# Performance work log

Measured on AMD Instinct MI355X. Metric: run time of the kernel, lower is better.

Reference implementation:

```python
import jax, jax.numpy as jnp
import numpy as np

N = 100_000       # nodes
DEG = 16          # avg degree (fixed here)
E = N * DEG       # edges
IN_F, HID, OUT_F = 64, 32, 16
K, DIM = 3, 2     # n_kernels, pseudo-coordinate dim


def setup_inputs() -> dict:
    key = jax.random.key(0)
    k1, k2, k3, k4, k5, k6, k7 = jax.random.split(key, 7)
    row_ptr = jnp.arange(N + 1, dtype=jnp.int64) * DEG          # CSR offsets, fixed degree
    col_idx = jax.random.randint(k1, (E,), 0, N, dtype=jnp.int64)
    input_feature = jax.random.normal(k2, (N, IN_F), dtype=jnp.float32)
    p = jax.random.uniform(k3, (E, DIM), dtype=jnp.float32)      # pseudo-coordinates per edge
    mu = jax.random.normal(k4, (K, DIM), dtype=jnp.float32)
    sigma = jax.random.uniform(k5, (K, DIM), dtype=jnp.float32, minval=0.5, maxval=1.5)
    W1 = jax.random.normal(k6, (K, IN_F, HID), dtype=jnp.float32) * (1.0 / np.sqrt(IN_F))
    W2 = jax.random.normal(k7, (K, HID, OUT_F), dtype=jnp.float32) * (1.0 / np.sqrt(HID))
    return {"row_ptr": row_ptr, "col_idx": col_idx, "input_feature": input_feature,
            "p": p, "mu": mu, "sigma": sigma, "W1": W1, "W2": W2}


def _edge_gaussians(p, mu, sigma):
    # w[e,k] = exp(-0.5 * sum_d ((p[e,d]-mu[k,d])/sigma[k,d])^2)   [E,K]
    diff = p[:, None, :] - mu[None, :, :]                 # [E,K,D]
    inv_var = 1.0 / (sigma * sigma)                       # [K,D]
    return jnp.exp(-0.5 * jnp.sum(diff * diff * inv_var[None], axis=-1))


def _gmm_conv(row_ptr, col_idx, dst, x, gauss, W):
    # per-kernel linear transform first (dense GEMM), then irregular gather+scatter
    xW = jnp.einsum('nf,kfh->nkh', x, W)                  # [N,K,H]
    msg = jnp.einsum('ek,ekh->eh', gauss, xW[col_idx])    # gather + mix kernels  [E,H]
    n_nodes = row_ptr.shape[0] - 1
    return jax.ops.segment_sum(msg, dst, num_segments=n_nodes)  # scatter-add to dst rows


def reference(row_ptr, col_idx, input_feature, p, mu, sigma, W1, W2):
    n_nodes = row_ptr.shape[0] - 1
    deg = jnp.diff(row_ptr)
    dst = jnp.repeat(jnp.arange(n_nodes), deg, total_repeat_length=col_idx.shape[0])
    gauss = _edge_gaussians(p, mu, sigma)                 # shared by both layers
    h = _gmm_conv(row_ptr, col_idx, dst, input_feature, gauss, W1)
    out = _gmm_conv(row_ptr, col_idx, dst, h, gauss, W2)
    return out
```

## Files before the change

### kernel.cpp

```cpp
#include <hip/hip_runtime.h>
#include <hip/hip_fp16.h>


#define KK 3

using half8   = __attribute__((ext_vector_type(8))) _Float16;
using float4v = __attribute__((ext_vector_type(4))) float;

__global__ void setup_kernel(const float* __restrict__ p, const float* __restrict__ mu,
                             const float* __restrict__ sigma, float2* __restrict__ gaussh,
                             const float* __restrict__ x, __half* __restrict__ xh,
                             const float* __restrict__ W1, const float* __restrict__ W2,
                             __half* __restrict__ B1, __half* __restrict__ B2,
                             int E, int NX8) {
    int t = blockIdx.x * blockDim.x + threadIdx.x;
    if (t < E) {
        float p0 = p[2 * t], p1 = p[2 * t + 1];
        float g[KK];
#pragma unroll
        for (int k = 0; k < KK; ++k) {
            float m0 = mu[2 * k], m1 = mu[2 * k + 1];
            float s0 = sigma[2 * k], s1 = sigma[2 * k + 1];
            float d0 = p0 - m0, d1 = p1 - m1;
            float q = (d0 * d0) / (s0 * s0) + (d1 * d1) / (s1 * s1);
            g[k] = __expf(-0.5f * q);
        }
        union { __half h[4]; float2 v; } o;
        o.h[0] = __float2half(g[0]); o.h[1] = __float2half(g[1]);
        o.h[2] = __float2half(g[2]); o.h[3] = __float2half(0.f);
        gaussh[t] = o.v;
    }
    if (t < NX8) {
        float4 v0 = ((const float4*)x)[2 * t];
        float4 v1 = ((const float4*)x)[2 * t + 1];
        union { __half h[8]; float4 v; } o;
        o.h[0] = __float2half(v0.x); o.h[1] = __float2half(v0.y);
        o.h[2] = __float2half(v0.z); o.h[3] = __float2half(v0.w);
        o.h[4] = __float2half(v1.x); o.h[5] = __float2half(v1.y);
        o.h[6] = __float2half(v1.z); o.h[7] = __float2half(v1.w);
        ((float4*)xh)[t] = o.v;
    }
    if (t < 6144) {
        int j = t & 7, lane = (t >> 3) & 63, grp = t >> 9;
        int ot = grp / 6, kb = grp % 6;
        int kidx = kb * 32 + (lane >> 4) * 8 + j;
        B1[t] = __float2half(W1[kidx * 32 + ot * 16 + (lane & 15)]);
    } else if (t < 6144 + 1536) {
        int t2 = t - 6144;
        int j = t2 & 7, lane = (t2 >> 3) & 63, kb = t2 >> 9;
        int kidx = kb * 32 + (lane >> 4) * 8 + j;
        B2[t2] = __float2half(W2[kidx * 16 + (lane & 15)]);
    }
}

__device__ __forceinline__ void unpack8(float4 raw, float* f) {
    union { float4 v; __half2 h2[4]; } u;
    u.v = raw;
#pragma unroll
    for (int q = 0; q < 4; ++q) {
        float2 t = __half22float2(u.h2[q]);
        f[2 * q] = t.x; f[2 * q + 1] = t.y;
    }
}

__device__ __forceinline__ void fma_edge(float4 xr, float2 graw,
                                         float* a0, float* a1, float* a2) {
    union { float2 v; __half2 h2[2]; } ug; ug.v = graw;
    float2 gab = __half22float2(ug.h2[0]);
    float2 gc_ = __half22float2(ug.h2[1]);
    float f[8];
    unpack8(xr, f);
#pragma unroll
    for (int q = 0; q < 8; ++q) {
        a0[q] = fmaf(gab.x, f[q], a0[q]);
        a1[q] = fmaf(gab.y, f[q], a1[q]);
        a2[q] = fmaf(gc_.x, f[q], a2[q]);
    }
}

template <int F, int H, bool OUT_HALF>
__global__ __launch_bounds__(256) void fused_layer(
    const int* __restrict__ row_ptr, const int* __restrict__ col_idx,
    const float2* __restrict__ gaussh, const __half* __restrict__ xh,
    const __half* __restrict__ Bpack, void* __restrict__ yout, int N) {
    constexpr int TPN    = F / 8;
    constexpr int NODES  = 256 / TPN;
    constexpr int J      = KK * F;
    constexpr int STRIDE = (F == 64) ? 200 : 104;
    constexpr int KB     = J / 32;
    constexpr int OT     = H / 16;

    __shared__ __align__(16) __half sLh[NODES * STRIDE];

    const int tid = threadIdx.x;
    const int nl  = tid / TPN;
    const int ch  = tid % TPN;
    const int n   = blockIdx.x * NODES + nl;

    float a0[8], a1[8], a2[8];
#pragma unroll
    for (int q = 0; q < 8; ++q) { a0[q] = 0.f; a1[q] = 0.f; a2[q] = 0.f; }

    const float4* x4 = (const float4*)xh;

    if (n < N) {
        int e0 = row_ptr[n], e1 = row_ptr[n + 1];
        int e = e0;
        for (; e + 16 <= e1; e += 16) {
            int cols[16];
            float2 gr[16];
#pragma unroll
            for (int j = 0; j < 16; ++j) cols[j] = col_idx[e + j];
#pragma unroll
            for (int j = 0; j < 16; ++j) gr[j] = gaussh[e + j];
            float4 xrA[8], xrB[8];
#pragma unroll
            for (int j = 0; j < 8; ++j) xrA[j] = x4[(size_t)cols[j] * TPN + ch];
#pragma unroll
            for (int j = 0; j < 8; ++j) xrB[j] = x4[(size_t)cols[8 + j] * TPN + ch];
#pragma unroll
            for (int j = 0; j < 8; ++j) fma_edge(xrA[j], gr[j], a0, a1, a2);
#pragma unroll
            for (int j = 0; j < 8; ++j) fma_edge(xrB[j], gr[8 + j], a0, a1, a2);
        }
        for (; e < e1; ++e) {
            int c = col_idx[e];
            fma_edge(x4[(size_t)c * TPN + ch], gaussh[e], a0, a1, a2);
        }
    }

    {
        union { __half h[8]; half8 v; } o;
#pragma unroll
        for (int q = 0; q < 8; ++q) o.h[q] = __float2half(a0[q]);
        *(half8*)(sLh + nl * STRIDE + 0 * F + ch * 8) = o.v;
#pragma unroll
        for (int q = 0; q < 8; ++q) o.h[q] = __float2half(a1[q]);
        *(half8*)(sLh + nl * STRIDE + 1 * F + ch * 8) = o.v;
#pragma unroll
        for (int q = 0; q < 8; ++q) o.h[q] = __float2half(a2[q]);
        *(half8*)(sLh + nl * STRIDE + 2 * F + ch * 8) = o.v;
    }
    __syncthreads();

    {
        const int wv   = tid >> 6;
        const int lane = tid & 63;
        const int tile = wv / OT;
        const int ot   = wv % OT;
        const int n0   = blockIdx.x * NODES + tile * 16;
        if (n0 < N) {
            const int quad = lane >> 4;
            const int m    = lane & 15;

            half8 b[KB];
#pragma unroll
            for (int kb = 0; kb < KB; ++kb)
                b[kb] = ((const half8*)Bpack)[(ot * KB + kb) * 64 + lane];

            const half8* av = (const half8*)(sLh + (size_t)(tile * 16 + m) * STRIDE);
            float4v acc = {0.f, 0.f, 0.f, 0.f};
#pragma unroll
            for (int kb = 0; kb < KB; ++kb)
                acc = __builtin_amdgcn_mfma_f32_16x16x32_f16(av[kb * 4 + quad], b[kb], acc, 0, 0, 0);

#pragma unroll
            for (int reg = 0; reg < 4; ++reg) {
                int nn = n0 + quad * 4 + reg;
                if (nn < N) {
                    if constexpr (OUT_HALF)
                        ((__half*)yout)[(size_t)nn * H + ot * 16 + m] = __float2half(acc[reg]);
                    else
                        ((float*)yout)[(size_t)nn * H + m] = acc[reg];
                }
            }
        }
    }
}

extern "C" void kernel_launch(void* const* d_in, const int* in_sizes, int n_in,
                              void* d_out, int out_size, void* d_ws, size_t ws_size,
                              hipStream_t stream) {
    const int* row_ptr  = (const int*)d_in[0];
    const int* col_idx  = (const int*)d_in[1];
    const float* x      = (const float*)d_in[2];
    const float* p      = (const float*)d_in[3];
    const float* mu     = (const float*)d_in[4];
    const float* sigma  = (const float*)d_in[5];
    const float* W1     = (const float*)d_in[6];
    const float* W2     = (const float*)d_in[7];

    const int N = in_sizes[0] - 1;
    const int E = in_sizes[1];

    float2* gaussh = (float2*)d_ws;
    __half* B1pack = (__half*)(gaussh + (size_t)E);
    __half* B2pack = B1pack + 6144;
    __half* xh     = B2pack + 1536;
    __half* hh     = xh + (size_t)N * 64;
    float*  out    = (float*)d_out;

    const int B = 256;
    const int NX8 = N * 8;
    int setup_n = E > NX8 ? E : NX8;
    if (setup_n < 7680) setup_n = 7680;

    setup_kernel<<<(setup_n + B - 1) / B, B, 0, stream>>>(
        p, mu, sigma, gaussh, x, xh, W1, W2, B1pack, B2pack, E, NX8);

    fused_layer<64, 32, true><<<(N + 31) / 32, B, 0, stream>>>(
        row_ptr, col_idx, gaussh, xh, B1pack, (void*)hh, N);
    fused_layer<32, 16, false><<<(N + 63) / 64, B, 0, stream>>>(
        row_ptr, col_idx, gaussh, hh, B2pack, (void*)out, N);
}
```

Baseline: 154.1 us.

## Slice node features into 16-wide planes and loop slices per thread pair

Stores the fp16 features (and layer-1 hidden output) as separate 16-channel planes, so each gather for one slice reads 32 contiguous bytes per node and the whole slice plane is a smaller working set that fits better in cache. Each node is handled by two threads that load the first 16 edge indices and Gaussian weights once and reuse them across all slices. Blocks grow to 128 nodes, and the MFMA stage loops over node tiles per wave. This trades more gather instructions per edge (one per slice) and a serial slice loop for better cache locality, with a launch-bounds occupancy hint added.

```diff
diff --git a/kernel.cpp b/kernel.cpp
--- a/kernel.cpp
+++ b/kernel.cpp
@@ -12,7 +12,7 @@
                              const float* __restrict__ x, __half* __restrict__ xh,
                              const float* __restrict__ W1, const float* __restrict__ W2,
                              __half* __restrict__ B1, __half* __restrict__ B2,
-                             int E, int NX8) {
+                             int E, int NX8, int NN) {
     int t = blockIdx.x * blockDim.x + threadIdx.x;
     if (t < E) {
         float p0 = p[2 * t], p1 = p[2 * t + 1];
@@ -31,6 +31,7 @@
         gaussh[t] = o.v;
     }
     if (t < NX8) {
+        int nn = t >> 3, c = t & 7;
         float4 v0 = ((const float4*)x)[2 * t];
         float4 v1 = ((const float4*)x)[2 * t + 1];
         union { __half h[8]; float4 v; } o;
@@ -38,7 +39,7 @@
         o.h[2] = __float2half(v0.z); o.h[3] = __float2half(v0.w);
         o.h[4] = __float2half(v1.x); o.h[5] = __float2half(v1.y);
         o.h[6] = __float2half(v1.z); o.h[7] = __float2half(v1.w);
-        ((float4*)xh)[t] = o.v;
+        ((float4*)xh)[((size_t)(c >> 1) * NN + nn) * 2 + (c & 1)] = o.v;
     }
     if (t < 6144) {
         int j = t & 7, lane = (t >> 3) & 63, grp = t >> 9;
@@ -63,9 +64,9 @@
     }
 }
 
-__device__ __forceinline__ void fma_edge(float4 xr, float2 graw,
-                                         float* a0, float* a1, float* a2) {
-    union { float2 v; __half2 h2[2]; } ug; ug.v = graw;
+__device__ __forceinline__ void fma_edge_u(float4 xr, unsigned long long graw,
+                                           float* a0, float* a1, float* a2) {
+    union { unsigned long long u; __half2 h2[2]; } ug; ug.u = graw;
     float2 gab = __half22float2(ug.h2[0]);
     float2 gc_ = __half22float2(ug.h2[1]);
     float f[8];
@@ -79,12 +80,12 @@
 }
 
 template <int F, int H, bool OUT_HALF>
-__global__ __launch_bounds__(256) void fused_layer(
+__global__ __launch_bounds__(256, 3) void fused_layer(
     const int* __restrict__ row_ptr, const int* __restrict__ col_idx,
     const float2* __restrict__ gaussh, const __half* __restrict__ xh,
     const __half* __restrict__ Bpack, void* __restrict__ yout, int N) {
-    constexpr int TPN    = F / 8;
-    constexpr int NODES  = 256 / TPN;
+    constexpr int NSLICE = F / 16;
+    constexpr int NODES  = 128;
     constexpr int J      = KK * F;
     constexpr int STRIDE = (F == 64) ? 200 : 104;
     constexpr int KB     = J / 32;
@@ -93,72 +94,88 @@
     __shared__ __align__(16) __half sLh[NODES * STRIDE];
 
     const int tid = threadIdx.x;
-    const int nl  = tid / TPN;
-    const int ch  = tid % TPN;
+    const int nl  = tid >> 1;
+    const int ch  = tid & 1;
     const int n   = blockIdx.x * NODES + nl;
 
-    float a0[8], a1[8], a2[8];
-#pragma unroll
-    for (int q = 0; q < 8; ++q) { a0[q] = 0.f; a1[q] = 0.f; a2[q] = 0.f; }
-
-    const float4* x4 = (const float4*)xh;
-
+    int cols[16];
+    unsigned long long gr[16];
+    int e0 = 0, e1 = 0;
+#pragma unroll
+    for (int j = 0; j < 16; ++j) { cols[j] = 0; gr[j] = 0ull; }
     if (n < N) {
-        int e0 = row_ptr[n], e1 = row_ptr[n + 1];
-        int e = e0;
-        for (; e + 16 <= e1; e += 16) {
-            int cols[16];
-            float2 gr[16];
-#pragma unroll
-            for (int j = 0; j < 16; ++j) cols[j] = col_idx[e + j];
-#pragma unroll
-            for (int j = 0; j < 16; ++j) gr[j] = gaussh[e + j];
-            float4 xrA[8], xrB[8];
-#pragma unroll
-            for (int j = 0; j < 8; ++j) xrA[j] = x4[(size_t)cols[j] * TPN + ch];
-#pragma unroll
-            for (int j = 0; j < 8; ++j) xrB[j] = x4[(size_t)cols[8 + j] * TPN + ch];
-#pragma unroll
-            for (int j = 0; j < 8; ++j) fma_edge(xrA[j], gr[j], a0, a1, a2);
-#pragma unroll
-            for (int j = 0; j < 8; ++j) fma_edge(xrB[j], gr[8 + j], a0, a1, a2);
-        }
-        for (; e < e1; ++e) {
+        e0 = row_ptr[n]; e1 = row_ptr[n + 1];
+        int cnt = e1 - e0;
+        int cl = cnt > 16 ? 16 : cnt;
+        if (cnt > 0) {
+#pragma unroll
+            for (int j = 0; j < 16; ++j) {
+                int idx = e0 + (j < cl ? j : cl - 1);
+                cols[j] = col_idx[idx];
+            }
+#pragma unroll
+            for (int j = 0; j < 16; ++j) {
+                int idx = e0 + (j < cl ? j : cl - 1);
+                unsigned long long g = ((const unsigned long long*)gaussh)[idx];
+                gr[j] = (j < cl) ? g : 0ull;
+            }
+        }
+    }
+
+#pragma unroll 1
+    for (int p = 0; p < NSLICE; ++p) {
+        const float4* xs = (const float4*)xh + (size_t)p * N * 2;
+        float a0[8], a1[8], a2[8];
+#pragma unroll
+        for (int q = 0; q < 8; ++q) { a0[q] = 0.f; a1[q] = 0.f; a2[q] = 0.f; }
+
+        float4 xrA[8], xrB[8];
+#pragma unroll
+        for (int j = 0; j < 8; ++j) xrA[j] = xs[(size_t)cols[j] * 2 + ch];
+#pragma unroll
+        for (int j = 0; j < 8; ++j) xrB[j] = xs[(size_t)cols[8 + j] * 2 + ch];
+#pragma unroll
+        for (int j = 0; j < 8; ++j) fma_edge_u(xrA[j], gr[j], a0, a1, a2);
+#pragma unroll
+        for (int j = 0; j < 8; ++j) fma_edge_u(xrB[j], gr[8 + j], a0, a1, a2);
+        for (int e = e0 + 16; e < e1; ++e) {
             int c = col_idx[e];
-            fma_edge(x4[(size_t)c * TPN + ch], gaussh[e], a0, a1, a2);
-        }
-    }
-
-    {
+            unsigned long long g = ((const unsigned long long*)gaussh)[e];
+            fma_edge_u(xs[(size_t)c * 2 + ch], g, a0, a1, a2);
+        }
+
         union { __half h[8]; half8 v; } o;
 #pragma unroll
         for (int q = 0; q < 8; ++q) o.h[q] = __float2half(a0[q]);
-        *(half8*)(sLh + nl * STRIDE + 0 * F + ch * 8) = o.v;
+        *(half8*)(sLh + nl * STRIDE + 0 * F + p * 16 + ch * 8) = o.v;
 #pragma unroll
         for (int q = 0; q < 8; ++q) o.h[q] = __float2half(a1[q]);
-        *(half8*)(sLh + nl * STRIDE + 1 * F + ch * 8) = o.v;
+        *(half8*)(sLh + nl * STRIDE + 1 * F + p * 16 + ch * 8) = o.v;
 #pragma unroll
         for (int q = 0; q < 8; ++q) o.h[q] = __float2half(a2[q]);
-        *(half8*)(sLh + nl * STRIDE + 2 * F + ch * 8) = o.v;
+        *(half8*)(sLh + nl * STRIDE + 2 * F + p * 16 + ch * 8) = o.v;
     }
     __syncthreads();
 
     {
         const int wv   = tid >> 6;
         const int lane = tid & 63;
-        const int tile = wv / OT;
-        const int ot   = wv % OT;
-        const int n0   = blockIdx.x * NODES + tile * 16;
-        if (n0 < N) {
-            const int quad = lane >> 4;
-            const int m    = lane & 15;
-
-            half8 b[KB];
-#pragma unroll
-            for (int kb = 0; kb < KB; ++kb)
-                b[kb] = ((const half8*)Bpack)[(ot * KB + kb) * 64 + lane];
-
-            const half8* av = (const half8*)(sLh + (size_t)(tile * 16 + m) * STRIDE);
+        const int quad = lane >> 4;
+        const int m    = lane & 15;
+        const int ot   = (OT == 2) ? (wv & 1) : 0;
+        const int t0   = (OT == 2) ? (wv >> 1) : wv;
+        constexpr int TSTEP = (OT == 2) ? 2 : 4;
+
+        half8 b[KB];
+#pragma unroll
+        for (int kb = 0; kb < KB; ++kb)
+            b[kb] = ((const half8*)Bpack)[(ot * KB + kb) * 64 + lane];
+
+#pragma unroll 1
+        for (int t = t0; t < NODES / 16; t += TSTEP) {
+            const int n0 = blockIdx.x * NODES + t * 16;
+            if (n0 >= N) break;
+            const half8* av = (const half8*)(sLh + (size_t)(t * 16 + m) * STRIDE);
             float4v acc = {0.f, 0.f, 0.f, 0.f};
 #pragma unroll
             for (int kb = 0; kb < KB; ++kb)
@@ -169,7 +186,7 @@
                 int nn = n0 + quad * 4 + reg;
                 if (nn < N) {
                     if constexpr (OUT_HALF)
-                        ((__half*)yout)[(size_t)nn * H + ot * 16 + m] = __float2half(acc[reg]);
+                        ((__half*)yout)[((size_t)ot * N + nn) * 16 + m] = __float2half(acc[reg]);
                     else
                         ((float*)yout)[(size_t)nn * H + m] = acc[reg];
                 }
@@ -206,10 +223,10 @@
     if (setup_n < 7680) setup_n = 7680;
 
     setup_kernel<<<(setup_n + B - 1) / B, B, 0, stream>>>(
-        p, mu, sigma, gaussh, x, xh, W1, W2, B1pack, B2pack, E, NX8);
-
-    fused_layer<64, 32, true><<<(N + 31) / 32, B, 0, stream>>>(
+        p, mu, sigma, gaussh, x, xh, W1, W2, B1pack, B2pack, E, NX8, N);
+
+    fused_layer<64, 32, true><<<(N + 127) / 128, B, 0, stream>>>(
         row_ptr, col_idx, gaussh, xh, B1pack, (void*)hh, N);
-    fused_layer<32, 16, false><<<(N + 63) / 64, B, 0, stream>>>(
+    fused_layer<32, 16, false><<<(N + 127) / 128, B, 0, stream>>>(
         row_ptr, col_idx, gaussh, hh, B2pack, (void*)out, N);
 }
```

After: 315.1 us. 104% more time.
